# Kernel tuning notes

Measured on AMD Instinct MI355X. Metric: run time of the kernel, lower is better.

## Reference

```python
import jax, jax.numpy as jnp
import numpy as np

B, S, D, H = 2, 2048, 1024, 16
HD = D // H  # head_dim = 64
ROPE_BASE = 10000.0
INIT_STD = 0.02


def setup_inputs() -> dict:
    key = jax.random.key(0)
    k1, k2, k3 = jax.random.split(key, 3)
    x = jax.random.normal(k1, (B, S, D), dtype=jnp.float32)
    w_qkv = jax.random.normal(k2, (3 * D, D), dtype=jnp.float32) * INIT_STD
    w_out = jax.random.normal(k3, (D, D), dtype=jnp.float32) * (1.0 / np.sqrt(D))
    b_out = jnp.zeros((D,), dtype=jnp.float32)
    return {"x": x, "w_qkv": w_qkv, "w_out": w_out, "b_out": b_out}


def _rope_cos_sin(s_len, head_dim, dtype):
    theta = 1.0 / ROPE_BASE ** (jnp.arange(0, head_dim, 2, dtype=jnp.float32) / head_dim)
    freqs = jnp.outer(jnp.arange(s_len, dtype=jnp.float32), theta)  # [s, d/2]
    freqs = jnp.concatenate([freqs, freqs], axis=-1)  # [s, d]
    return jnp.cos(freqs).astype(dtype), jnp.sin(freqs).astype(dtype)


def _apply_rope(qk, cos, sin):
    # qk: [b, h, s, d]; rotate-half: (-x2, x1)
    d2 = qk.shape[-1] // 2
    x1, x2 = qk[..., :d2], qk[..., d2:]
    rot = jnp.concatenate([-x2, x1], axis=-1)
    return qk * cos + rot * sin


def reference(x, w_qkv, w_out, b_out):
    b, s, d = x.shape
    qkv = jnp.einsum('bsd,ed->bse', x, w_qkv)  # [b, s, 3D]
    qkv = qkv.reshape(b, s, 3 * H, HD).transpose(0, 2, 1, 3)  # [b, 3h, s, d]
    qk, v = qkv[:, :2 * H], qkv[:, 2 * H:]
    cos, sin = _rope_cos_sin(s, HD, x.dtype)
    qk = _apply_rope(qk, cos, sin)
    q, k = qk[:, :H], qk[:, H:]
    scale = 1.0 / np.sqrt(HD)
    scores = jnp.einsum('bhqd,bhkd->bhqk', q, k) * scale  # [b, h, s, s]
    causal = jnp.tril(jnp.ones((s, s), dtype=bool))
    scores = jnp.where(causal, scores, jnp.finfo(scores.dtype).min)
    attn = jax.nn.softmax(scores, axis=-1)
    o = jnp.einsum('bhqk,bhkd->bhqd', attn, v)  # [b, h, s, d]
    o = o.transpose(0, 2, 1, 3).reshape(b, s, d)
    return jnp.einsum('bsd,ed->bse', o, w_out) + b_out
```

## Files before the change

### kernel.cpp

```cpp
#include <hip/hip_runtime.h>
#include <hip/hip_fp16.h>
#include <math.h>

#define B_  2
#define S_  2048
#define D_  1024
#define H_  16
#define HD_ 64

typedef _Float16  f16;
typedef __attribute__((ext_vector_type(8))) _Float16 f16x8;
typedef __attribute__((ext_vector_type(4))) _Float16 f16x4;
typedef __attribute__((ext_vector_type(4))) float    f32x4;

#define LOG2E 1.4426950408889634f
#define L2_10000_DIV32 0.41524101186092029f

__device__ __forceinline__ float fin(float v) { return (v == v) ? v : 0.0f; }

__device__ __forceinline__ f16x8 cvt8(const float* p) {
  float4 a = *(const float4*)p;
  float4 b = *(const float4*)(p + 4);
  f16x8 h;
  h[0] = (f16)a.x; h[1] = (f16)a.y; h[2] = (f16)a.z; h[3] = (f16)a.w;
  h[4] = (f16)b.x; h[5] = (f16)b.y; h[6] = (f16)b.z; h[7] = (f16)b.w;
  return h;
}

__device__ __forceinline__ int swz64(int r, int c) {
  return r * 64 + ((((c >> 3) ^ (r & 7)) << 3) | (c & 7));
}

#define GLD16(g, l)                                                        \
  __builtin_amdgcn_global_load_lds(                                        \
      (const __attribute__((address_space(1))) void*)(g),                  \
      (__attribute__((address_space(3))) void*)(l), 16, 0, 0)

__global__ void __launch_bounds__(256)
k_cvt3(const float* __restrict__ wq, const float* __restrict__ wo,
       const float* __restrict__ x,
       f16* __restrict__ wqh, f16* __restrict__ woh, f16* __restrict__ xh,
       float2* __restrict__ tab, int doX)
{
  const int NWQ = 3 * D_ * D_ / 4, NWO = D_ * D_ / 4, NX = B_ * S_ * D_ / 4;
  const int n = NWQ + NWO + (doX ? NX : 0);
  for (int i = blockIdx.x * 256 + threadIdx.x; i < n; i += gridDim.x * 256) {
    const float* src; f16* dst; int j;
    if (i < NWQ)            { src = wq; dst = wqh; j = i; }
    else if (i < NWQ + NWO) { src = wo; dst = woh; j = i - NWQ; }
    else                    { src = x;  dst = xh;  j = i - NWQ - NWO; }
    float4 v = ((const float4*)src)[j];
    f16x4 h = {(f16)v.x, (f16)v.y, (f16)v.z, (f16)v.w};
    ((f16x4*)dst)[j] = h;
  }
  for (int i = blockIdx.x * 256 + threadIdx.x; i < S_ * 32; i += gridDim.x * 256) {
    const int p = i >> 5, j = i & 31;
    const float th = exp2f(-(float)j * L2_10000_DIV32);
    float s, c;
    sincosf((float)p * th, &s, &c);
    tab[i] = make_float2(c, s);
  }
}

template <bool XF16>
__global__ void __launch_bounds__(256)
k_qkv3(const float* __restrict__ xf, const f16* __restrict__ xh,
       const f16* __restrict__ wqh, const float2* __restrict__ tab,
       f16* __restrict__ Qb, f16* __restrict__ Kb, f16* __restrict__ Vt)
{
  __shared__ __align__(16) f16 As[128 * 64];
  __shared__ __align__(16) f16 Bs[128 * 64];
  const int t = threadIdx.x;
  const int w = t >> 6;
  const int lane = t & 63;
  const int ll = lane & 15;
  const int quad = lane >> 4;
  const int wm = w >> 1, wn = w & 1;
  const int row0 = blockIdx.y * 128;
  const int col0 = blockIdx.x * 128;

  const f32x4 fz = {0.f, 0.f, 0.f, 0.f};
  f32x4 acc[4][4];
#pragma unroll
  for (int i = 0; i < 4; ++i)
#pragma unroll
    for (int j = 0; j < 4; ++j) acc[i][j] = fz;

  const int rO = lane >> 3;
  const int gc = (lane & 7) ^ rO;
  const f16* gah2 = xh  + (size_t)(row0 + w * 8 + rO) * D_ + gc * 8;
  const f16* gb2  = wqh + (size_t)(col0 + w * 8 + rO) * D_ + gc * 8;

  const int ldr = t >> 3;
  const int ldk = (t & 7) * 8;
  const float* gaf = xf + (size_t)(row0 + ldr) * D_ + ldk;

  for (int kt = 0; kt < D_; kt += 64) {
    f16x8 ra[4];
    if (!XF16) {
#pragma unroll
      for (int i = 0; i < 4; ++i)
        ra[i] = cvt8(gaf + (size_t)i * 32 * D_ + kt);
    }
    __syncthreads();
    if (XF16) {
#pragma unroll
      for (int i = 0; i < 4; ++i) {
        GLD16(gah2 + (size_t)(i * 32) * D_ + kt, &As[(i * 32 + w * 8) * 64]);
        GLD16(gb2  + (size_t)(i * 32) * D_ + kt, &Bs[(i * 32 + w * 8) * 64]);
      }
    } else {
#pragma unroll
      for (int i = 0; i < 4; ++i) {
        *(f16x8*)&As[swz64(i * 32 + ldr, ldk)] = ra[i];
        GLD16(gb2 + (size_t)(i * 32) * D_ + kt, &Bs[(i * 32 + w * 8) * 64]);
      }
    }
    __syncthreads();
#pragma unroll
    for (int kk = 0; kk < 64; kk += 32) {
      f16x8 a[4], b[4];
#pragma unroll
      for (int mt = 0; mt < 4; ++mt)
        a[mt] = *(const f16x8*)&As[swz64(wm * 64 + mt * 16 + ll, kk + quad * 8)];
#pragma unroll
      for (int nt = 0; nt < 4; ++nt)
        b[nt] = *(const f16x8*)&Bs[swz64(wn * 64 + nt * 16 + ll, kk + quad * 8)];
#pragma unroll
      for (int mt = 0; mt < 4; ++mt)
#pragma unroll
        for (int nt = 0; nt < 4; ++nt)
          acc[mt][nt] = __builtin_amdgcn_mfma_f32_16x16x32_f16(
              a[mt], b[nt], acc[mt][nt], 0, 0, 0);
    }
  }

  const int h3 = (col0 >> 6) + wn;
  if (h3 < 32) {
    f16* dst = (h3 < 16) ? Qb : Kb;
    const int h = (h3 < 16) ? h3 : h3 - 16;
#pragma unroll
    for (int mt = 0; mt < 4; ++mt) {
#pragma unroll
      for (int r = 0; r < 4; ++r) {
        const int row = row0 + wm * 64 + mt * 16 + quad * 4 + r;
        const int b = row >> 11;
        const int p = row & (S_ - 1);
        f16* base = dst + ((size_t)(b * H_ + h) * S_ + p) * HD_;
        const float2 cs0 = tab[p * 32 + ll];
        const float2 cs1 = tab[p * 32 + 16 + ll];
        {
          float x1 = acc[mt][0][r], x2 = acc[mt][2][r];
          base[ll]      = (f16)fin(x1 * cs0.x - x2 * cs0.y);
          base[ll + 32] = (f16)fin(x2 * cs0.x + x1 * cs0.y);
        }
        {
          float x1 = acc[mt][1][r], x2 = acc[mt][3][r];
          base[16 + ll]      = (f16)fin(x1 * cs1.x - x2 * cs1.y);
          base[16 + ll + 32] = (f16)fin(x2 * cs1.x + x1 * cs1.y);
        }
      }
    }
  } else {
    const int hv = h3 - 32;
#pragma unroll
    for (int mt = 0; mt < 4; ++mt)
#pragma unroll
      for (int nt = 0; nt < 4; ++nt)
#pragma unroll
        for (int r = 0; r < 4; ++r) {
          const int row = row0 + wm * 64 + mt * 16 + quad * 4 + r;
          const int b = row >> 11;
          const int p = row & (S_ - 1);
          const int dd = nt * 16 + ll;
          Vt[((size_t)(b * H_ + hv) * HD_ + dd) * S_ + p] = (f16)fin(acc[mt][nt][r]);
        }
  }
}

__device__ __forceinline__ bool softmax_tile7(
    f32x4 sc[4], bool diag, int qloc, int quad,
    float& mrun, float& lrun, float& alpha, f16* const pst[4])
{
  if (diag) {
#pragma unroll
    for (int nt = 0; nt < 4; ++nt)
#pragma unroll
      for (int r = 0; r < 4; ++r)
        if ((nt * 16 + quad * 4 + r) > qloc) sc[nt][r] = -3.0e4f;
  }
  float pm = mrun;
#pragma unroll
  for (int nt = 0; nt < 4; ++nt)
#pragma unroll
    for (int r = 0; r < 4; ++r) pm = fmaxf(pm, sc[nt][r]);
  pm = fmaxf(pm, __shfl_xor(pm, 16));
  pm = fmaxf(pm, __shfl_xor(pm, 32));
  const bool resc = !__all(pm <= mrun + 8.0f);
  if (resc) { alpha = exp2f(mrun - pm); mrun = pm; }
  float ps = 0.f;
#pragma unroll
  for (int nt = 0; nt < 4; ++nt) {
    f16x4 pk;
#pragma unroll
    for (int r = 0; r < 4; ++r) {
      float p = exp2f(sc[nt][r] - mrun);
      ps += p;
      pk[r] = (f16)p;
    }
    *(f16x4*)pst[nt] = pk;
  }
  ps += __shfl_xor(ps, 16);
  ps += __shfl_xor(ps, 32);
  lrun = (resc ? lrun * alpha : lrun) + ps;
  return resc;
}

__device__ __forceinline__ void write_o7(
    f32x4 acco[4], float lrun, f16* const pst[4],
    const f16* pb0, const f16* pb1,
    int ll, int quad, int w, int qt, size_t bh, f16* Ob)
{
  const float inv = 1.0f / fmaxf(lrun, 1e-30f);
#pragma unroll
  for (int dg = 0; dg < 4; ++dg) {
    f16x4 ov;
#pragma unroll
    for (int r = 0; r < 4; ++r) ov[r] = (f16)fin(acco[dg][r] * inv);
    *(f16x4*)pst[dg] = ov;
  }
  const size_t row = bh * S_ + qt * 64 + w * 16 + ll;
  f16x8 o0 = *(const f16x8*)pb0;
  f16x8 o1 = *(const f16x8*)pb1;
  *(f16x8*)&Ob[row * HD_ + quad * 8]      = o0;
  *(f16x8*)&Ob[row * HD_ + 32 + quad * 8] = o1;
}

#define ABODY(KB0, KB1, VB0, VB1, WKA, WKB, WVA, WVB, PRE, DIAG)           \
  do {                                                                     \
    f16x8 nk0, nk1, nv0, nv1;                                              \
    if (PRE) {                                                             \
      nk0 = *(const f16x8*)pK; nk1 = *(const f16x8*)(pK + 8);              \
    }                                                                      \
    f16x8 ak[2][4];                                                        \
    _Pragma("unroll")                                                      \
    for (int nt = 0; nt < 4; ++nt) {                                       \
      ak[0][nt] = *(const f16x8*)(KB0 + nt * 1024);                        \
      ak[1][nt] = *(const f16x8*)(KB1 + nt * 1024);                        \
    }                                                                      \
    f32x4 s[4] = {fz, fz, fz, fz};                                         \
    __builtin_amdgcn_s_setprio(1);                                         \
    _Pragma("unroll")                                                      \
    for (int k2 = 0; k2 < 2; ++k2)                                         \
      _Pragma("unroll")                                                    \
      for (int nt = 0; nt < 4; ++nt)                                       \
        s[nt] = __builtin_amdgcn_mfma_f32_16x16x32_f16(                    \
            ak[k2][nt], bq[k2], s[nt], 0, 0, 0);                           \
    __builtin_amdgcn_s_setprio(0);                                         \
    if (PRE) {                                                             \
      nv0 = *(const f16x8*)pV; nv1 = *(const f16x8*)(pV + 8);              \
      pK += 64 * HD_; pV += 64;                                            \
    }                                                                      \
    float alpha;                                                           \
    const bool resc = softmax_tile7(s, DIAG, qloc, quad, m, l, alpha, pst);\
    if (resc) {                                                            \
      _Pragma("unroll")                                                    \
      for (int dg = 0; dg < 4; ++dg)                                       \
        _Pragma("unroll")                                                  \
        for (int r = 0; r < 4; ++r) acco[dg][r] *= alpha;                  \
    }                                                                      \
    f16x8 av[2][4];                                                        \
    _Pragma("unroll")                                                      \
    for (int dg = 0; dg < 4; ++dg) {                                       \
      av[0][dg] = *(const f16x8*)(VB0 + dg * 1024);                        \
      av[1][dg] = *(const f16x8*)(VB1 + dg * 1024);                        \
    }                                                                      \
    f16x8 bp0 = *(const f16x8*)pb0;                                        \
    f16x8 bp1 = *(const f16x8*)pb1;                                        \
    __builtin_amdgcn_s_setprio(1);                                         \
    _Pragma("unroll")                                                      \
    for (int dg = 0; dg < 4; ++dg)                                         \
      acco[dg] = __builtin_amdgcn_mfma_f32_16x16x32_f16(                   \
          av[0][dg], bp0, acco[dg], 0, 0, 0);                              \
    _Pragma("unroll")                                                      \
    for (int dg = 0; dg < 4; ++dg)                                         \
      acco[dg] = __builtin_amdgcn_mfma_f32_16x16x32_f16(                   \
          av[1][dg], bp1, acco[dg], 0, 0, 0);                              \
    __builtin_amdgcn_s_setprio(0);                                         \
    if (PRE) {                                                             \
      *(f16x8*)WKA = nk0; *(f16x8*)WKB = nk1;                              \
      *(f16x8*)WVA = nv0; *(f16x8*)WVB = nv1;                              \
    }                                                                      \
    __syncthreads();                                                       \
  } while (0)

#define ABODY_B0(PRE, DIAG) \
  ABODY(kb00, kb01, vb00, vb01, wk1a, wk1b, wv1a, wv1b, PRE, DIAG)
#define ABODY_B1(PRE, DIAG) \
  ABODY(kb10, kb11, vb10, vb11, wk0a, wk0b, wv0a, wv0b, PRE, DIAG)

__global__ void __launch_bounds__(256, 4)
k_attn7(const f16* Qb, const f16* __restrict__ Kb,
        const f16* __restrict__ Vt, f16* Ob)
{
  __shared__ __align__(16) f16 Ks[2][64 * 64];
  __shared__ __align__(16) f16 Vs[2][64 * 64];
  __shared__ __align__(16) f16 Ps[4][16 * 64];

  const int t = threadIdx.x;
  const int w = t >> 6;
  const int lane = t & 63;
  const int ll = lane & 15;
  const int quad = lane >> 4;
  const int bx = blockIdx.x;
  const int base = (bx & 1) ? 31 - (bx >> 1) : (bx >> 1);
  const int qt = ((int)blockIdx.y < 8) ? base : 31 - base;
  const int h = blockIdx.y;
  const int b = blockIdx.z;
  const size_t bh = (size_t)b * H_ + h;
  const f16* Qg = Qb + bh * S_ * HD_;
  const f16* Kg = Kb + bh * S_ * HD_;
  const f16* Vg = Vt + bh * HD_ * S_;

  f16x8 bq[2];
  {
    const f16 hsc = (f16)(0.125f * LOG2E);
#pragma unroll
    for (int k2 = 0; k2 < 2; ++k2) {
      bq[k2] = *(const f16x8*)(Qg + (size_t)(qt * 64 + w * 16 + ll) * HD_ + k2 * 32 + quad * 8);
#pragma unroll
      for (int e = 0; e < 8; ++e) bq[k2][e] *= hsc;
    }
  }

  f16* Pt = &Ps[w][0];
  const f16* kb00 = &Ks[0][swz64(ll, quad * 8)];
  const f16* kb01 = &Ks[0][swz64(ll, 32 + quad * 8)];
  const f16* kb10 = &Ks[1][swz64(ll, quad * 8)];
  const f16* kb11 = &Ks[1][swz64(ll, 32 + quad * 8)];
  const f16* vb00 = &Vs[0][swz64(ll, quad * 8)];
  const f16* vb01 = &Vs[0][swz64(ll, 32 + quad * 8)];
  const f16* vb10 = &Vs[1][swz64(ll, quad * 8)];
  const f16* vb11 = &Vs[1][swz64(ll, 32 + quad * 8)];
  const f16* pb0  = &Pt[swz64(ll, quad * 8)];
  const f16* pb1  = &Pt[swz64(ll, 32 + quad * 8)];
  f16* pst[4] = { &Pt[swz64(ll, 0 * 16 + quad * 4)],
                  &Pt[swz64(ll, 1 * 16 + quad * 4)],
                  &Pt[swz64(ll, 2 * 16 + quad * 4)],
                  &Pt[swz64(ll, 3 * 16 + quad * 4)] };
  const int sr = t >> 2;
  const int scc = (t & 3) * 16;
  f16* wk0a = &Ks[0][swz64(sr, scc)];
  f16* wk0b = &Ks[0][swz64(sr, scc + 8)];
  f16* wk1a = &Ks[1][swz64(sr, scc)];
  f16* wk1b = &Ks[1][swz64(sr, scc + 8)];
  f16* wv0a = &Vs[0][swz64(sr, scc)];
  f16* wv0b = &Vs[0][swz64(sr, scc + 8)];
  f16* wv1a = &Vs[1][swz64(sr, scc)];
  f16* wv1b = &Vs[1][swz64(sr, scc + 8)];

  {
    f16x8 a0 = *(const f16x8*)(Kg + (size_t)sr * HD_ + scc);
    f16x8 a1 = *(const f16x8*)(Kg + (size_t)sr * HD_ + scc + 8);
    f16x8 b0 = *(const f16x8*)(Vg + (size_t)sr * S_ + scc);
    f16x8 b1 = *(const f16x8*)(Vg + (size_t)sr * S_ + scc + 8);
    *(f16x8*)wk0a = a0;
    *(f16x8*)wk0b = a1;
    *(f16x8*)wv0a = b0;
    *(f16x8*)wv0b = b1;
  }
  __syncthreads();

  const f16* pK = Kg + (size_t)(64 + sr) * HD_ + scc;
  const f16* pV = Vg + (size_t)sr * S_ + 64 + scc;

  const f32x4 fz = {0.f, 0.f, 0.f, 0.f};
  f32x4 acco[4] = {fz, fz, fz, fz};
  float m = -3.0e4f, l = 0.f;
  const int qloc = w * 16 + ll;

  int j = 0;
  while (j + 1 < qt) {
    ABODY_B0(true, false);
    ABODY_B1(true, false);
    j += 2;
  }
  if (j < qt) {
    ABODY_B0(true, false);
    ++j;
    ABODY_B1(false, true);
  } else {
    ABODY_B0(false, true);
  }

  write_o7(acco, l, pst, pb0, pb1, ll, quad, w, qt, bh, Ob);
}

__global__ void __launch_bounds__(256)
k_out3(const f16* __restrict__ Ob, const f16* __restrict__ Wh,
       const float* __restrict__ bias, float* __restrict__ out)
{
  __shared__ __align__(16) f16 As[64 * 64];
  __shared__ __align__(16) f16 Bs[128 * 64];
  const int t = threadIdx.x;
  const int w = t >> 6;
  const int lane = t & 63;
  const int ll = lane & 15;
  const int quad = lane >> 4;
  const int wm = w >> 1, wn = w & 1;
  const int row0 = blockIdx.y * 64;
  const int col0 = blockIdx.x * 128;
  const int bb = row0 >> 11;
  const int s0 = row0 & (S_ - 1);

  const f32x4 fz = {0.f, 0.f, 0.f, 0.f};
  f32x4 acc[2][4];
#pragma unroll
  for (int i = 0; i < 2; ++i)
#pragma unroll
    for (int j = 0; j < 4; ++j) acc[i][j] = fz;

  const int rO = lane >> 3;
  const int gc = (lane & 7) ^ rO;
  const f16* gb2 = Wh + (size_t)(col0 + w * 8 + rO) * D_ + gc * 8;

  for (int kt = 0; kt < 16; ++kt) {
    const f16* ga2 = Ob + (((size_t)(bb * H_ + kt)) * S_ + s0 + w * 8 + rO) * HD_ + gc * 8;
    __syncthreads();
#pragma unroll
    for (int i = 0; i < 2; ++i)
      GLD16(ga2 + (size_t)(i * 32) * HD_, &As[(i * 32 + w * 8) * 64]);
#pragma unroll
    for (int i = 0; i < 4; ++i)
      GLD16(gb2 + (size_t)(i * 32) * D_ + kt * 64, &Bs[(i * 32 + w * 8) * 64]);
    __syncthreads();
#pragma unroll
    for (int kk = 0; kk < 64; kk += 32) {
      f16x8 a[2], b[4];
#pragma unroll
      for (int mt = 0; mt < 2; ++mt)
        a[mt] = *(const f16x8*)&As[swz64(wm * 32 + mt * 16 + ll, kk + quad * 8)];
#pragma unroll
      for (int nt = 0; nt < 4; ++nt)
        b[nt] = *(const f16x8*)&Bs[swz64(wn * 64 + nt * 16 + ll, kk + quad * 8)];
#pragma unroll
      for (int mt = 0; mt < 2; ++mt)
#pragma unroll
        for (int nt = 0; nt < 4; ++nt)
          acc[mt][nt] = __builtin_amdgcn_mfma_f32_16x16x32_f16(
              a[mt], b[nt], acc[mt][nt], 0, 0, 0);
    }
  }

#pragma unroll
  for (int mt = 0; mt < 2; ++mt)
#pragma unroll
    for (int r = 0; r < 4; ++r) {
      const int row = row0 + wm * 32 + mt * 16 + quad * 4 + r;
#pragma unroll
      for (int nt = 0; nt < 4; ++nt) {
        const int col = col0 + wn * 64 + nt * 16 + ll;
        out[(size_t)row * D_ + col] = fin(acc[mt][nt][r] + bias[col]);
      }
    }
}

extern "C" void kernel_launch(void* const* d_in, const int* in_sizes, int n_in,
                              void* d_out, int out_size, void* d_ws, size_t ws_size,
                              hipStream_t stream) {
  const float* x    = (const float*)d_in[0];
  const float* wqkv = (const float*)d_in[1];
  const float* wout = (const float*)d_in[2];
  const float* bout = (const float*)d_in[3];
  float* out = (float*)d_out;

  char* ws = (char*)d_ws;
  f16* wqh = (f16*)(ws);
  f16* Qb  = (f16*)(ws + 6291456);
  f16* Kb  = (f16*)(ws + 14680064);
  f16* Vt  = (f16*)(ws + 23068672);
  f16* woh = (f16*)(ws + 31457280);
  const bool bigws = ws_size >= (size_t)41943040;
  f16* xh  = (f16*)(ws + 33554432);

  float2* tab = (float2*)((char*)d_out + 9437184);

  k_cvt3<<<2048, 256, 0, stream>>>(wqkv, wout, x, wqh, woh, xh, tab, bigws ? 1 : 0);
  if (bigws)
    k_qkv3<true><<<dim3(3 * D_ / 128, (B_ * S_) / 128), 256, 0, stream>>>(
        x, xh, wqh, tab, Qb, Kb, Vt);
  else
    k_qkv3<false><<<dim3(3 * D_ / 128, (B_ * S_) / 128), 256, 0, stream>>>(
        x, xh, wqh, tab, Qb, Kb, Vt);
  k_attn7<<<dim3(32, H_, B_), 256, 0, stream>>>(Qb, Kb, Vt, Qb );
  k_out3<<<dim3(D_ / 128, (B_ * S_) / 64), 256, 0, stream>>>(
      Qb, woh, bout, out);
}
```

Measured before the change: 182.5 us.

## Double-buffer LDS tiles in QKV and output projection GEMMs

Adds two-stage LDS buffering to the QKV projection (f16 path) and the output projection kernels. The next K-slice is loaded asynchronously while MFMAs run on the current one, which removes one barrier per iteration. Swizzled read offsets are precomputed outside the loop. LDS use per block doubles (64KB for the QKV kernel), which may lower occupancy.

```diff
diff --git a/kernel.cpp b/kernel.cpp
--- a/kernel.cpp
+++ b/kernel.cpp
@@ -64,12 +64,12 @@
 
 template <bool XF16>
 __global__ void __launch_bounds__(256)
-k_qkv3(const float* __restrict__ xf, const f16* __restrict__ xh,
+k_qkv4(const float* __restrict__ xf, const f16* __restrict__ xh,
        const f16* __restrict__ wqh, const float2* __restrict__ tab,
        f16* __restrict__ Qb, f16* __restrict__ Kb, f16* __restrict__ Vt)
 {
-  __shared__ __align__(16) f16 As[128 * 64];
-  __shared__ __align__(16) f16 Bs[128 * 64];
+  __shared__ __align__(16) f16 As[2][128 * 64];
+  __shared__ __align__(16) f16 Bs[2][128 * 64];
   const int t = threadIdx.x;
   const int w = t >> 6;
   const int lane = t & 63;
@@ -88,50 +88,88 @@
 
   const int rO = lane >> 3;
   const int gc = (lane & 7) ^ rO;
-  const f16* gah2 = xh  + (size_t)(row0 + w * 8 + rO) * D_ + gc * 8;
-  const f16* gb2  = wqh + (size_t)(col0 + w * 8 + rO) * D_ + gc * 8;
+  const f16* pA = xh  + (size_t)(row0 + w * 8 + rO) * D_ + gc * 8;
+  const f16* pB = wqh + (size_t)(col0 + w * 8 + rO) * D_ + gc * 8;
+  const int ldst = (w * 8) * 64;
+
+  const int raA0 = swz64(ll, quad * 8);
+  const int raA1 = swz64(ll, 32 + quad * 8);
 
   const int ldr = t >> 3;
   const int ldk = (t & 7) * 8;
   const float* gaf = xf + (size_t)(row0 + ldr) * D_ + ldk;
 
-  for (int kt = 0; kt < D_; kt += 64) {
-    f16x8 ra[4];
-    if (!XF16) {
+  if (XF16) {
+#pragma unroll
+    for (int i = 0; i < 4; ++i) {
+      GLD16(pA + (size_t)(i * 32) * D_, &As[0][i * 32 * 64 + ldst]);
+      GLD16(pB + (size_t)(i * 32) * D_, &Bs[0][i * 32 * 64 + ldst]);
+    }
+    __syncthreads();
+    pA += 64; pB += 64;
+
+    for (int kt = 0; kt < 16; ++kt) {
+      const int cur = kt & 1, nxt = cur ^ 1;
+      if (kt < 15) {
+#pragma unroll
+        for (int i = 0; i < 4; ++i) {
+          GLD16(pA + (size_t)(i * 32) * D_, &As[nxt][i * 32 * 64 + ldst]);
+          GLD16(pB + (size_t)(i * 32) * D_, &Bs[nxt][i * 32 * 64 + ldst]);
+        }
+        pA += 64; pB += 64;
+      }
+      const f16* Ac = &As[cur][0];
+      const f16* Bc = &Bs[cur][0];
+#pragma unroll
+      for (int kk = 0; kk < 2; ++kk) {
+        const int ro = kk ? raA1 : raA0;
+        f16x8 a[4], b[4];
+#pragma unroll
+        for (int mt = 0; mt < 4; ++mt)
+          a[mt] = *(const f16x8*)&Ac[(wm * 64 + mt * 16) * 64 + ro];
+#pragma unroll
+        for (int nt = 0; nt < 4; ++nt)
+          b[nt] = *(const f16x8*)&Bc[(wn * 64 + nt * 16) * 64 + ro];
+#pragma unroll
+        for (int mt = 0; mt < 4; ++mt)
+#pragma unroll
+          for (int nt = 0; nt < 4; ++nt)
+            acc[mt][nt] = __builtin_amdgcn_mfma_f32_16x16x32_f16(
+                a[mt], b[nt], acc[mt][nt], 0, 0, 0);
+      }
+      __syncthreads();
+    }
+  } else {
+    for (int kt = 0; kt < D_; kt += 64) {
+      f16x8 ra[4];
 #pragma unroll
       for (int i = 0; i < 4; ++i)
         ra[i] = cvt8(gaf + (size_t)i * 32 * D_ + kt);
-    }
-    __syncthreads();
-    if (XF16) {
+      __syncthreads();
 #pragma unroll
       for (int i = 0; i < 4; ++i) {
-        GLD16(gah2 + (size_t)(i * 32) * D_ + kt, &As[(i * 32 + w * 8) * 64]);
-        GLD16(gb2  + (size_t)(i * 32) * D_ + kt, &Bs[(i * 32 + w * 8) * 64]);
+        *(f16x8*)&As[0][swz64(i * 32 + ldr, ldk)] = ra[i];
+        GLD16(pB + (size_t)(i * 32) * D_ + kt, &Bs[0][i * 32 * 64 + ldst]);
       }
-    } else {
-#pragma unroll
-      for (int i = 0; i < 4; ++i) {
-        *(f16x8*)&As[swz64(i * 32 + ldr, ldk)] = ra[i];
-        GLD16(gb2 + (size_t)(i * 32) * D_ + kt, &Bs[(i * 32 + w * 8) * 64]);
+      __syncthreads();
+#pragma unroll
+      for (int kk = 0; kk < 2; ++kk) {
+        const int ro = kk ? raA1 : raA0;
+        f16x8 a[4], b[4];
+#pragma unroll
+        for (int mt = 0; mt < 4; ++mt)
+          a[mt] = *(const f16x8*)&As[0][(wm * 64 + mt * 16) * 64 + ro];
+#pragma unroll
+        for (int nt = 0; nt < 4; ++nt)
+          b[nt] = *(const f16x8*)&Bs[0][(wn * 64 + nt * 16) * 64 + ro];
+#pragma unroll
+        for (int mt = 0; mt < 4; ++mt)
+#pragma unroll
+          for (int nt = 0; nt < 4; ++nt)
+            acc[mt][nt] = __builtin_amdgcn_mfma_f32_16x16x32_f16(
+                a[mt], b[nt], acc[mt][nt], 0, 0, 0);
       }
-    }
-    __syncthreads();
-#pragma unroll
-    for (int kk = 0; kk < 64; kk += 32) {
-      f16x8 a[4], b[4];
-#pragma unroll
-      for (int mt = 0; mt < 4; ++mt)
-        a[mt] = *(const f16x8*)&As[swz64(wm * 64 + mt * 16 + ll, kk + quad * 8)];
-#pragma unroll
-      for (int nt = 0; nt < 4; ++nt)
-        b[nt] = *(const f16x8*)&Bs[swz64(wn * 64 + nt * 16 + ll, kk + quad * 8)];
-#pragma unroll
-      for (int mt = 0; mt < 4; ++mt)
-#pragma unroll
-        for (int nt = 0; nt < 4; ++nt)
-          acc[mt][nt] = __builtin_amdgcn_mfma_f32_16x16x32_f16(
-              a[mt], b[nt], acc[mt][nt], 0, 0, 0);
+      __syncthreads();
     }
   }
 
@@ -397,11 +435,11 @@
 }
 
 __global__ void __launch_bounds__(256)
-k_out3(const f16* __restrict__ Ob, const f16* __restrict__ Wh,
+k_out4(const f16* __restrict__ Ob, const f16* __restrict__ Wh,
        const float* __restrict__ bias, float* __restrict__ out)
 {
-  __shared__ __align__(16) f16 As[64 * 64];
-  __shared__ __align__(16) f16 Bs[128 * 64];
+  __shared__ __align__(16) f16 As[2][64 * 64];
+  __shared__ __align__(16) f16 Bs[2][128 * 64];
   const int t = threadIdx.x;
   const int w = t >> 6;
   const int lane = t & 63;
@@ -422,27 +460,47 @@
 
   const int rO = lane >> 3;
   const int gc = (lane & 7) ^ rO;
-  const f16* gb2 = Wh + (size_t)(col0 + w * 8 + rO) * D_ + gc * 8;
+  const int ldst = (w * 8) * 64;
+  const f16* pB = Wh + (size_t)(col0 + w * 8 + rO) * D_ + gc * 8;
+  const f16* pA = Ob + (((size_t)(bb * H_)) * S_ + s0 + w * 8 + rO) * HD_ + gc * 8;
+
+  const int raA0 = swz64(ll, quad * 8);
+  const int raA1 = swz64(ll, 32 + quad * 8);
+
+#pragma unroll
+  for (int i = 0; i < 2; ++i)
+    GLD16(pA + (size_t)(i * 32) * HD_, &As[0][i * 32 * 64 + ldst]);
+#pragma unroll
+  for (int i = 0; i < 4; ++i)
+    GLD16(pB + (size_t)(i * 32) * D_, &Bs[0][i * 32 * 64 + ldst]);
+  __syncthreads();
+  pA += (size_t)S_ * HD_;
+  pB += 64;
 
   for (int kt = 0; kt < 16; ++kt) {
-    const f16* ga2 = Ob + (((size_t)(bb * H_ + kt)) * S_ + s0 + w * 8 + rO) * HD_ + gc * 8;
-    __syncthreads();
-#pragma unroll
-    for (int i = 0; i < 2; ++i)
-      GLD16(ga2 + (size_t)(i * 32) * HD_, &As[(i * 32 + w * 8) * 64]);
-#pragma unroll
-    for (int i = 0; i < 4; ++i)
-      GLD16(gb2 + (size_t)(i * 32) * D_ + kt * 64, &Bs[(i * 32 + w * 8) * 64]);
-    __syncthreads();
-#pragma unroll
-    for (int kk = 0; kk < 64; kk += 32) {
+    const int cur = kt & 1, nxt = cur ^ 1;
+    if (kt < 15) {
+#pragma unroll
+      for (int i = 0; i < 2; ++i)
+        GLD16(pA + (size_t)(i * 32) * HD_, &As[nxt][i * 32 * 64 + ldst]);
+#pragma unroll
+      for (int i = 0; i < 4; ++i)
+        GLD16(pB + (size_t)(i * 32) * D_, &Bs[nxt][i * 32 * 64 + ldst]);
+      pA += (size_t)S_ * HD_;
+      pB += 64;
+    }
+    const f16* Ac = &As[cur][0];
+    const f16* Bc = &Bs[cur][0];
+#pragma unroll
+    for (int kk = 0; kk < 2; ++kk) {
+      const int ro = kk ? raA1 : raA0;
       f16x8 a[2], b[4];
 #pragma unroll
       for (int mt = 0; mt < 2; ++mt)
-        a[mt] = *(const f16x8*)&As[swz64(wm * 32 + mt * 16 + ll, kk + quad * 8)];
+        a[mt] = *(const f16x8*)&Ac[(wm * 32 + mt * 16) * 64 + ro];
 #pragma unroll
       for (int nt = 0; nt < 4; ++nt)
-        b[nt] = *(const f16x8*)&Bs[swz64(wn * 64 + nt * 16 + ll, kk + quad * 8)];
+        b[nt] = *(const f16x8*)&Bc[(wn * 64 + nt * 16) * 64 + ro];
 #pragma unroll
       for (int mt = 0; mt < 2; ++mt)
 #pragma unroll
@@ -450,6 +508,7 @@
           acc[mt][nt] = __builtin_amdgcn_mfma_f32_16x16x32_f16(
               a[mt], b[nt], acc[mt][nt], 0, 0, 0);
     }
+    __syncthreads();
   }
 
 #pragma unroll
@@ -487,12 +546,12 @@
 
   k_cvt3<<<2048, 256, 0, stream>>>(wqkv, wout, x, wqh, woh, xh, tab, bigws ? 1 : 0);
   if (bigws)
-    k_qkv3<true><<<dim3(3 * D_ / 128, (B_ * S_) / 128), 256, 0, stream>>>(
+    k_qkv4<true><<<dim3(3 * D_ / 128, (B_ * S_) / 128), 256, 0, stream>>>(
         x, xh, wqh, tab, Qb, Kb, Vt);
   else
-    k_qkv3<false><<<dim3(3 * D_ / 128, (B_ * S_) / 128), 256, 0, stream>>>(
+    k_qkv4<false><<<dim3(3 * D_ / 128, (B_ * S_) / 128), 256, 0, stream>>>(
         x, xh, wqh, tab, Qb, Kb, Vt);
   k_attn7<<<dim3(32, H_, B_), 256, 0, stream>>>(Qb, Kb, Vt, Qb );
-  k_out3<<<dim3(D_ / 128, (B_ * S_) / 64), 256, 0, stream>>>(
+  k_out4<<<dim3(D_ / 128, (B_ * S_) / 64), 256, 0, stream>>>(
       Qb, woh, bout, out);
 }
```

Measured after the change: 201.9 us. 10.6% more time.
